# Kernel tuning notes

Measured on AMD Instinct MI355X. Metric: run time of the kernel, lower is better.

The kernel has to match this reference:

```python
import jax, jax.numpy as jnp
import numpy as np

N = 2048        # number of entities
D = 2048        # entity_dimensionality
HEADS = 16
HD = D // HEADS  # per-head dim = 128
ROUNDS = 2
LAYERS = 2


def setup_inputs() -> dict:
    key = jax.random.key(0)
    ks = jax.random.split(key, 12)
    s = 1.0 / np.sqrt(D)  # keep activations O(1)
    inp = {
        "entities": jax.random.normal(ks[0], (N, D), jnp.float32),
        "Wq": jax.random.normal(ks[1], (D, D), jnp.float32) * s,
        "bq": jnp.zeros((D,), jnp.float32),
        "Wk": jax.random.normal(ks[2], (D, D), jnp.float32) * s,
        "bk": jnp.zeros((D,), jnp.float32),
        "Wv": jax.random.normal(ks[3], (D, D), jnp.float32) * s,
        "bv": jnp.zeros((D,), jnp.float32),
        "W0": jax.random.normal(ks[4], (D, D), jnp.float32) * s,
        "b0": jnp.zeros((D,), jnp.float32),
        "W1": jax.random.normal(ks[5], (D, D), jnp.float32) * s,
        "b1": jnp.zeros((D,), jnp.float32),
    }
    return inp


def _linear(x, W, b):
    # torch nn.Linear: y = x @ W.T + b
    return x @ W.T + b


def _split_heads(x):
    # [N, D] -> [H, N, hd]
    return x.reshape(N, HEADS, HD).transpose(1, 0, 2)


def reference(entities, Wq, bq, Wk, bk, Wv, bv, W0, b0, W1, b1):
    scale = 1.0 / np.sqrt(HD)
    for _ in range(ROUNDS):
        q = _split_heads(_linear(entities, Wq, bq))  # [H, N, hd]
        k = _split_heads(_linear(entities, Wk, bk))
        v = _split_heads(_linear(entities, Wv, bv))
        scores = jnp.einsum('hqd,hkd->hqk', q, k) * scale  # [H, N, N]
        attn = jax.nn.softmax(scores, axis=-1)
        o = jnp.einsum('hqk,hkd->hqd', attn, v)            # [H, N, hd]
        o = o.transpose(1, 0, 2).reshape(N, D)             # merge heads
        o = jax.nn.relu(_linear(o, W0, b0))
        o = jax.nn.relu(_linear(o, W1, b1))
        entities = entities + o  # residual=True
    return entities
```

## Files before the change

kernel.cpp:

```cpp
#include <hip/hip_runtime.h>
#include <stdint.h>

#define DIM   2048
#define NENT  2048
#define NHEAD 16
#define HD    128

typedef unsigned short u16;
typedef u16   u16x4  __attribute__((ext_vector_type(4)));
typedef u16   u16x8  __attribute__((ext_vector_type(8)));
typedef float f32x4  __attribute__((ext_vector_type(4)));
typedef float f32x16 __attribute__((ext_vector_type(16)));
typedef __bf16 bf16x8 __attribute__((ext_vector_type(8)));

#define MFMA16(a, b, c) __builtin_amdgcn_mfma_f32_16x16x32_bf16((a), (b), (c), 0, 0, 0)
#define MFMA32(a, b, c) __builtin_amdgcn_mfma_f32_32x32x16_bf16((a), (b), (c), 0, 0, 0)

#define SMUL 0.12751743f

__device__ __forceinline__ u16 f2b(float f) {
  union { float f; unsigned int u; } x; x.f = f;
  unsigned int r = x.u + 0x7FFFu + ((x.u >> 16) & 1u);
  return (u16)(r >> 16);
}
__device__ __forceinline__ float b2f(u16 b) {
  union { unsigned int u; float f; } x; x.u = ((unsigned int)b) << 16;
  return x.f;
}
__device__ __forceinline__ unsigned int cvtpk(float a, float b) {
  unsigned int r;
  asm("v_cvt_pk_bf16_f32 %0, %1, %2" : "=v"(r) : "v"(a), "v"(b));
  return r;
}
__device__ __forceinline__ float exp2_fast(float x) {
  float r;
  asm("v_exp_f32 %0, %1" : "=v"(r) : "v"(x));
  return r;
}

__device__ __forceinline__ void async16(const void* g, void* l) {
  __builtin_amdgcn_global_load_lds(
      (const __attribute__((address_space(1))) unsigned int*)(uintptr_t)g,
      (__attribute__((address_space(3))) unsigned int*)(uintptr_t)l, 16, 0, 0);
}

__global__ void __launch_bounds__(256) conv6_k(
    const float* __restrict__ s0, const float* __restrict__ s1,
    const float* __restrict__ s2, const float* __restrict__ s3,
    const float* __restrict__ s4, const float* __restrict__ s5,
    u16* __restrict__ d0, u16* __restrict__ d1, u16* __restrict__ d2,
    u16* __restrict__ d3, u16* __restrict__ d4, u16* __restrict__ d5) {
  int sel = blockIdx.y;
  const float* s = sel == 0 ? s0 : sel == 1 ? s1 : sel == 2 ? s2
                 : sel == 3 ? s3 : sel == 4 ? s4 : s5;
  u16* d = sel == 0 ? d0 : sel == 1 ? d1 : sel == 2 ? d2
         : sel == 3 ? d3 : sel == 4 ? d4 : d5;
  int i = blockIdx.x * 256 + threadIdx.x;
  float4 v = ((const float4*)s)[i];
  u16x4 o;
  o.x = f2b(v.x); o.y = f2b(v.y); o.z = f2b(v.z); o.w = f2b(v.w);
  *(u16x4*)(d + (size_t)i * 4) = o;
}

template <int MODE>
__device__ __forceinline__ void gemm128_body(
    u16* sbuf,
    const u16* __restrict__ A, const u16* __restrict__ Bw,
    const float* __restrict__ bias, u16* __restrict__ C,
    int brow0, int bcol0, int kbase, int NT, float oscale) {
  u16* lA = sbuf;
  u16* lB = sbuf + 8192;
  const int tid = threadIdx.x;
  const int lane = tid & 63, w = tid >> 6;
  const int wr = w >> 1, wc = w & 1;
  const int l15 = lane & 15;
  const int koff = (lane >> 4) * 8;
  const int swz = (l15 & 7) << 3;

  f32x4 acc[4][4];
#pragma unroll
  for (int m = 0; m < 4; m++)
#pragma unroll
    for (int n = 0; n < 4; n++) acc[m][n] = (f32x4)0.f;

  const int lr = w * 8 + (lane >> 3);
  const int scol = ((lane & 7) ^ (lr & 7)) * 8;

#pragma unroll 1
  for (int kt = 0; kt < NT; kt++) {
    const int colg = kbase + kt * 64 + scol;
#pragma unroll
    for (int i = 0; i < 4; i++) {
      async16(A + (size_t)(brow0 + i * 32 + lr) * DIM + colg,
              lA + i * 2048 + w * 512);
      async16(Bw + (size_t)(bcol0 + i * 32 + lr) * DIM + colg,
              lB + i * 2048 + w * 512);
    }
    __syncthreads();
#pragma unroll
    for (int kk = 0; kk < 2; kk++) {
      bf16x8 af[4], bfr[4];
#pragma unroll
      for (int m = 0; m < 4; m++)
        af[m] = *(const bf16x8*)(lA + (wr * 64 + m * 16 + l15) * 64 +
                                 ((kk * 32 + koff) ^ swz));
#pragma unroll
      for (int n = 0; n < 4; n++)
        bfr[n] = *(const bf16x8*)(lB + (wc * 64 + n * 16 + l15) * 64 +
                                  ((kk * 32 + koff) ^ swz));
#pragma unroll
      for (int m = 0; m < 4; m++)
#pragma unroll
        for (int n = 0; n < 4; n++)
          acc[m][n] = MFMA16(af[m], bfr[n], acc[m][n]);
    }
    __syncthreads();
  }

  if (MODE == 2) {
    u16* arena = sbuf + w * 4096;
#pragma unroll
    for (int n = 0; n < 4; n++) {
      int c_loc = n * 16 + l15;
      float bv = bias[bcol0 + wc * 64 + c_loc];
#pragma unroll
      for (int m = 0; m < 4; m++)
#pragma unroll
        for (int r = 0; r < 4; r++) {
          int r_loc = m * 16 + (lane >> 4) * 4 + r;
          arena[c_loc * 64 + (r_loc ^ ((c_loc & 7) * 8))] =
              f2b(acc[m][n][r] + bv);
        }
    }
    __syncthreads();
    const int h = (bcol0 + wc * 64) >> 7;
    const int d0 = (bcol0 + wc * 64) & 127;
    const int R0 = brow0 + wr * 64;
    u16* vbase = C + (size_t)h * HD * NENT + R0;
#pragma unroll
    for (int it = 0; it < 8; it++) {
      int d_loc = it * 8 + (lane >> 3);
      int r0 = (lane & 7) * 8;
      u16x8 val = *(const u16x8*)(arena + d_loc * 64 + (r0 ^ ((d_loc & 7) * 8)));
      *(u16x8*)(vbase + (size_t)(d0 + d_loc) * NENT + r0) = val;
    }
    return;
  }

#pragma unroll
  for (int n = 0; n < 4; n++) {
    int col = bcol0 + wc * 64 + n * 16 + l15;
    float bv = (MODE == 0) ? bias[col] : 0.f;
#pragma unroll
    for (int m = 0; m < 4; m++) {
#pragma unroll
      for (int r = 0; r < 4; r++) {
        int row = brow0 + wr * 64 + m * 16 + (lane >> 4) * 4 + r;
        float val = acc[m][n][r] + bv;
        if (MODE == 0) val *= oscale;
        C[(size_t)row * DIM + col] = f2b(val);
      }
    }
  }
}

__global__ void __launch_bounds__(256, 3) gemm128_qkv_k(
    const u16* __restrict__ A,
    const u16* __restrict__ Bq, const u16* __restrict__ Bk, const u16* __restrict__ Bv,
    const float* __restrict__ bq, const float* __restrict__ bk, const float* __restrict__ bv,
    u16* __restrict__ q, u16* __restrict__ k, u16* __restrict__ vt) {
  __shared__ u16 sbuf[2 * 128 * 64];
  int x = blockIdx.x & 7;
  int j = blockIdx.x >> 3;
  int bn48 = x * 6 + j % 6;
  int bm = j / 6;
  int sel = bn48 >> 4, bnn = bn48 & 15;
  if (sel == 2) {
    gemm128_body<2>(sbuf, A, Bv, bv, vt, bm * 128, bnn * 128, 0, 32, 1.f);
  } else {
    const u16* B = sel == 0 ? Bq : Bk;
    const float* bias = sel == 0 ? bq : bk;
    u16* Cc = sel == 0 ? q : k;
    gemm128_body<0>(sbuf, A, B, bias, Cc, bm * 128, bnn * 128, 0, 32,
                    sel == 0 ? SMUL : 1.f);
  }
}

__global__ void __launch_bounds__(256, 3) gemm128_sk3_k(
    const u16* __restrict__ A, const u16* __restrict__ Bw,
    u16* __restrict__ p0, u16* __restrict__ p1, u16* __restrict__ p2) {
  __shared__ u16 sbuf[2 * 128 * 64];
  int x = blockIdx.x & 7;
  int j = blockIdx.x >> 3;
  int rem = j % 6;
  int bn = 2 * x + (rem & 1);
  int sk = rem >> 1;
  int bm = j / 6;
  u16* part = sk == 0 ? p0 : (sk == 1 ? p1 : p2);
  int nt = (sk == 2) ? 10 : 11;
  gemm128_body<1>(sbuf, A, Bw, nullptr, part, bm * 128, bn * 128,
                  sk * 11 * 64, nt, 1.f);
}

template <int RESID>
__global__ void __launch_bounds__(256) reduce3_k(
    const u16* __restrict__ p0, const u16* __restrict__ p1,
    const u16* __restrict__ p2,
    const float* __restrict__ bias, const float* __restrict__ resid,
    float* __restrict__ outf, u16* __restrict__ outb) {
  int i = blockIdx.x * 256 + threadIdx.x;
  u16x8 a0 = ((const u16x8*)p0)[i];
  u16x8 a1 = ((const u16x8*)p1)[i];
  u16x8 a2 = ((const u16x8*)p2)[i];
  size_t base = (size_t)i * 8;
  int col = (int)(base & (DIM - 1));
  u16x8 ob;
  float of[8];
#pragma unroll
  for (int j = 0; j < 8; j++) {
    float s = b2f(a0[j]) + b2f(a1[j]) + b2f(a2[j]) + bias[col + j];
    s = fmaxf(s, 0.f);
    if (RESID) {
      float o = resid[base + j] + s;
      of[j] = o;
      ob[j] = f2b(o);
    } else {
      ob[j] = f2b(s);
    }
  }
  *(u16x8*)(outb + base) = ob;
  if (RESID) {
#pragma unroll
    for (int j = 0; j < 8; j++) outf[base + j] = of[j];
  }
}

__global__ void __launch_bounds__(256, 2) attn_k(
    const u16* __restrict__ q, const u16* __restrict__ kmat,
    const u16* __restrict__ vt, u16* __restrict__ oz0, u16* __restrict__ oz1,
    float* __restrict__ ml) {
  const int h = blockIdx.x, qb = blockIdx.y, kvs = blockIdx.z;
  u16* __restrict__ oz = kvs ? oz1 : oz0;
  __shared__ u16 lK[2][64 * 128];
  __shared__ u16 lV[2][128 * 64];
  const int tid = threadIdx.x, lane = tid & 63, w = tid >> 6;
  const int l31 = lane & 31, hl = lane >> 5;
  const int r4 = lane >> 4, r8 = lane >> 3;
  const int c16e = (lane & 15) * 8, c8e = (lane & 7) * 8;
  const int swz = (l31 & 7) << 3;
  const u16* vhead = vt + (size_t)h * HD * NENT;
  const int kv0 = kvs * (NENT / 2);

  const int qrow = qb * 128 + w * 32 + l31;
  const u16* qptr = q + (size_t)qrow * DIM + h * HD + hl * 8;
  bf16x8 qf[8];
#pragma unroll
  for (int ks = 0; ks < 8; ks++)
    qf[ks] = *(const bf16x8*)(qptr + ks * 16);

  auto stageKV = [&](int kt, int buf) {
    const size_t krow0 = (size_t)kv0 + kt * 64;
#pragma unroll
    for (int c = 0; c < 4; c++) {
      int ch = w * 4 + c;
      int krow = ch * 4 + r4;
      async16(kmat + (krow0 + krow) * DIM + h * HD + (c16e ^ ((krow & 7) << 3)),
              lK[buf] + ch * 512);
      int vrow = ch * 8 + r8;
      async16(vhead + (size_t)vrow * NENT + krow0 + (c8e ^ ((r8 & 7) << 3)),
              lV[buf] + ch * 512);
    }
  };

  f32x16 Oacc[4];
#pragma unroll
  for (int dt = 0; dt < 4; dt++) Oacc[dt] = (f32x16)0.f;
  float m_i = -1e30f, l_i = 0.f;

  stageKV(0, 0);
  int cur = 0;

#pragma unroll 1
  for (int kt = 0; kt < NENT / 2 / 64; kt++) {
    __syncthreads();
    if (kt + 1 < NENT / 2 / 64) stageKV(kt + 1, cur ^ 1);
    const u16* Kc = lK[cur];
    const u16* Vc = lV[cur];

    f32x16 sA = (f32x16)0.f, sB = (f32x16)0.f;
#pragma unroll
    for (int ks = 0; ks < 8; ks++) {
      bf16x8 a0 = *(const bf16x8*)(Kc + l31 * 128 + ((ks * 16 + hl * 8) ^ swz));
      sA = MFMA32(a0, qf[ks], sA);
      bf16x8 a1 = *(const bf16x8*)(Kc + (32 + l31) * 128 + ((ks * 16 + hl * 8) ^ swz));
      sB = MFMA32(a1, qf[ks], sB);
    }

    float pmax = sA[0];
#pragma unroll
    for (int i = 1; i < 16; i++) pmax = fmaxf(pmax, sA[i]);
#pragma unroll
    for (int i = 0; i < 16; i++) pmax = fmaxf(pmax, sB[i]);
    pmax = fmaxf(pmax, __shfl_xor(pmax, 32));
    bool resc = __any(pmax > m_i + 8.f);
    float corr = 1.f;
    if (resc) {
      float mn = fmaxf(m_i, pmax);
      corr = exp2_fast(m_i - mn);
      m_i = mn;
    }
    float ls = 0.f;
#pragma unroll
    for (int i = 0; i < 16; i++) { sA[i] = exp2_fast(sA[i] - m_i); ls += sA[i]; }
#pragma unroll
    for (int i = 0; i < 16; i++) { sB[i] = exp2_fast(sB[i] - m_i); ls += sB[i]; }
    l_i = l_i * corr + ls;
    if (resc) {
#pragma unroll
      for (int r = 0; r < 16; r++) {
        int qo = hl * 4 + (r & 3) + 8 * (r >> 2);
        float cr = __shfl(corr, qo);
        Oacc[0][r] *= cr; Oacc[1][r] *= cr; Oacc[2][r] *= cr; Oacc[3][r] *= cr;
      }
    }

#pragma unroll
    for (int ks = 0; ks < 4; ks++) {
      const f32x16& p = (ks < 2) ? sA : sB;
      const int E = ((2 * ks) & 3) * 4;
      const int Od = ((2 * ks + 1) & 3) * 4;
      unsigned int e0 = cvtpk(p[E + 0], p[E + 1]);
      unsigned int e1 = cvtpk(p[E + 2], p[E + 3]);
      unsigned int o0 = cvtpk(p[Od + 0], p[Od + 1]);
      unsigned int o1 = cvtpk(p[Od + 2], p[Od + 3]);
      asm volatile("v_permlane32_swap_b32 %0, %1" : "+v"(e0), "+v"(o0));
      asm volatile("v_permlane32_swap_b32 %0, %1" : "+v"(e1), "+v"(o1));
      union { unsigned int u[4]; bf16x8 v; } pk;
      pk.u[0] = e0; pk.u[1] = e1; pk.u[2] = o0; pk.u[3] = o1;
#pragma unroll
      for (int dt = 0; dt < 4; dt++) {
        bf16x8 b = *(const bf16x8*)(Vc + (dt * 32 + l31) * 64 +
                                    ((ks * 16 + hl * 8) ^ swz));
        Oacc[dt] = MFMA32(pk.v, b, Oacc[dt]);
      }
    }
    cur ^= 1;
  }

  float lt = l_i + __shfl_xor(l_i, 32);
  if (hl == 0) {
    float* mlp = ml + ((size_t)(kvs * NHEAD + h) * NENT + qrow) * 2;
    mlp[0] = m_i;
    mlp[1] = lt;
  }
#pragma unroll
  for (int r = 0; r < 16; r++) {
    int row = qb * 128 + w * 32 + hl * 4 + (r & 3) + 8 * (r >> 2);
#pragma unroll
    for (int dt = 0; dt < 4; dt++)
      oz[(size_t)row * DIM + h * HD + dt * 32 + l31] = f2b(Oacc[dt][r]);
  }
}

__global__ void __launch_bounds__(256) combine_k(
    const u16* __restrict__ O0, const u16* __restrict__ O1,
    const float* __restrict__ ml, u16* __restrict__ o) {
  int i = blockIdx.x * 256 + threadIdx.x;
  size_t base = (size_t)i * 8;
  int row = (int)(base >> 11);
  int h = ((int)base & (DIM - 1)) >> 7;
  const float* p0 = ml + ((size_t)h * NENT + row) * 2;
  const float* p1 = ml + ((size_t)(NHEAD + h) * NENT + row) * 2;
  float m0 = p0[0], l0 = p0[1];
  float m1 = p1[0], l1 = p1[1];
  float M = fmaxf(m0, m1);
  float w0 = exp2_fast(m0 - M), w1 = exp2_fast(m1 - M);
  float inv = 1.f / (l0 * w0 + l1 * w1);
  w0 *= inv; w1 *= inv;
  u16x8 a = ((const u16x8*)O0)[i], b = ((const u16x8*)O1)[i];
  u16x8 r;
#pragma unroll
  for (int j = 0; j < 8; j++) r[j] = f2b(b2f(a[j]) * w0 + b2f(b[j]) * w1);
  ((u16x8*)o)[i] = r;
}

extern "C" void kernel_launch(void* const* d_in, const int* in_sizes, int n_in,
                              void* d_out, int out_size, void* d_ws, size_t ws_size,
                              hipStream_t stream) {
  const float* ent_in = (const float*)d_in[0];
  const float* Wq = (const float*)d_in[1];
  const float* bq = (const float*)d_in[2];
  const float* Wk = (const float*)d_in[3];
  const float* bk = (const float*)d_in[4];
  const float* Wv = (const float*)d_in[5];
  const float* bv = (const float*)d_in[6];
  const float* W0 = (const float*)d_in[7];
  const float* b0 = (const float*)d_in[8];
  const float* W1 = (const float*)d_in[9];
  const float* b1 = (const float*)d_in[10];
  float* out = (float*)d_out;

  char* ws = (char*)d_ws;
  const size_t SZ = (size_t)DIM * DIM * 2;
  u16* wqb = (u16*)ws; ws += SZ;
  u16* wkb = (u16*)ws; ws += SZ;
  u16* wvb = (u16*)ws; ws += SZ;
  u16* w0b = (u16*)ws; ws += SZ;
  u16* w1b = (u16*)ws; ws += SZ;
  u16* entb = (u16*)ws; ws += SZ;
  u16* qb_ = (u16*)ws; ws += SZ;
  u16* kb_ = (u16*)ws; ws += SZ;
  u16* vb_ = (u16*)ws; ws += SZ;
  u16* vtb = (u16*)ws; ws += SZ;
  u16* ob_ = (u16*)ws; ws += SZ;
  u16* h1b = (u16*)ws; ws += SZ;

  conv6_k<<<dim3(4096, 6), 256, 0, stream>>>(Wq, Wk, Wv, W0, W1, ent_in,
                                             wqb, wkb, wvb, w0b, w1b, entb);

  for (int r = 0; r < 2; r++) {
    const float* cur = r ? (const float*)out : ent_in;
    gemm128_qkv_k<<<768, 256, 0, stream>>>(entb, wqb, wkb, wvb, bq, bk, bv,
                                           qb_, kb_, vtb);
    attn_k<<<dim3(16, 16, 2), 256, 0, stream>>>(qb_, kb_, vtb, vb_, h1b,
                                                (float*)entb);
    combine_k<<<2048, 256, 0, stream>>>(vb_, h1b, (const float*)entb, ob_);
    gemm128_sk3_k<<<768, 256, 0, stream>>>(ob_, w0b, entb, qb_, kb_);
    reduce3_k<0><<<2048, 256, 0, stream>>>(entb, qb_, kb_, b0, nullptr,
                                           nullptr, h1b);
    gemm128_sk3_k<<<768, 256, 0, stream>>>(h1b, w1b, entb, qb_, kb_);
    reduce3_k<1><<<2048, 256, 0, stream>>>(entb, qb_, kb_, b1, cur,
                                           out, entb);
  }
}
```

Measured before the change: 356.7 us.

## Split attention KV into three chunks, single-buffer LDS, raise occupancy

The attention kernel now splits the key/value range into three chunks (704/704/640 rows) instead of two, giving 768 blocks, and drops the double-buffered LDS staging in favour of a single buffer so three blocks can fit per CU. MFMA sections are wrapped in s_setprio to favour matrix issue across co-resident waves. The combine kernel merges three partial outputs, reusing ob_ as both the third partial and the output in place. The gain relies on occupancy and more blocks hiding load latency. The cost is losing the explicit prefetch overlap, adding an extra sync per tile, and more partial-output traffic in the combine step.

```diff
diff --git a/kernel.cpp b/kernel.cpp
--- a/kernel.cpp
+++ b/kernel.cpp
@@ -235,21 +235,22 @@
   }
 }
 
-__global__ void __launch_bounds__(256, 2) attn_k(
+__global__ void __launch_bounds__(256, 3) attn_k(
     const u16* __restrict__ q, const u16* __restrict__ kmat,
     const u16* __restrict__ vt, u16* __restrict__ oz0, u16* __restrict__ oz1,
-    float* __restrict__ ml) {
+    u16* __restrict__ oz2, float* __restrict__ ml) {
   const int h = blockIdx.x, qb = blockIdx.y, kvs = blockIdx.z;
-  u16* __restrict__ oz = kvs ? oz1 : oz0;
-  __shared__ u16 lK[2][64 * 128];
-  __shared__ u16 lV[2][128 * 64];
+  u16* __restrict__ oz = kvs == 0 ? oz0 : (kvs == 1 ? oz1 : oz2);
+  const int NT = (kvs == 2) ? 10 : 11;
+  const int kv0 = kvs * 704;
+  __shared__ u16 lK[64 * 128];
+  __shared__ u16 lV[128 * 64];
   const int tid = threadIdx.x, lane = tid & 63, w = tid >> 6;
   const int l31 = lane & 31, hl = lane >> 5;
   const int r4 = lane >> 4, r8 = lane >> 3;
   const int c16e = (lane & 15) * 8, c8e = (lane & 7) * 8;
   const int swz = (l31 & 7) << 3;
   const u16* vhead = vt + (size_t)h * HD * NENT;
-  const int kv0 = kvs * (NENT / 2);
 
   const int qrow = qb * 128 + w * 32 + l31;
   const u16* qptr = q + (size_t)qrow * DIM + h * HD + hl * 8;
@@ -258,43 +259,36 @@
   for (int ks = 0; ks < 8; ks++)
     qf[ks] = *(const bf16x8*)(qptr + ks * 16);
 
-  auto stageKV = [&](int kt, int buf) {
+  f32x16 Oacc[4];
+#pragma unroll
+  for (int dt = 0; dt < 4; dt++) Oacc[dt] = (f32x16)0.f;
+  float m_i = -1e30f, l_i = 0.f;
+
+#pragma unroll 1
+  for (int kt = 0; kt < NT; kt++) {
     const size_t krow0 = (size_t)kv0 + kt * 64;
 #pragma unroll
     for (int c = 0; c < 4; c++) {
       int ch = w * 4 + c;
       int krow = ch * 4 + r4;
       async16(kmat + (krow0 + krow) * DIM + h * HD + (c16e ^ ((krow & 7) << 3)),
-              lK[buf] + ch * 512);
+              lK + ch * 512);
       int vrow = ch * 8 + r8;
       async16(vhead + (size_t)vrow * NENT + krow0 + (c8e ^ ((r8 & 7) << 3)),
-              lV[buf] + ch * 512);
-    }
-  };
-
-  f32x16 Oacc[4];
-#pragma unroll
-  for (int dt = 0; dt < 4; dt++) Oacc[dt] = (f32x16)0.f;
-  float m_i = -1e30f, l_i = 0.f;
-
-  stageKV(0, 0);
-  int cur = 0;
-
-#pragma unroll 1
-  for (int kt = 0; kt < NENT / 2 / 64; kt++) {
+              lV + ch * 512);
+    }
     __syncthreads();
-    if (kt + 1 < NENT / 2 / 64) stageKV(kt + 1, cur ^ 1);
-    const u16* Kc = lK[cur];
-    const u16* Vc = lV[cur];
 
     f32x16 sA = (f32x16)0.f, sB = (f32x16)0.f;
+    __builtin_amdgcn_s_setprio(1);
 #pragma unroll
     for (int ks = 0; ks < 8; ks++) {
-      bf16x8 a0 = *(const bf16x8*)(Kc + l31 * 128 + ((ks * 16 + hl * 8) ^ swz));
+      bf16x8 a0 = *(const bf16x8*)(lK + l31 * 128 + ((ks * 16 + hl * 8) ^ swz));
       sA = MFMA32(a0, qf[ks], sA);
-      bf16x8 a1 = *(const bf16x8*)(Kc + (32 + l31) * 128 + ((ks * 16 + hl * 8) ^ swz));
+      bf16x8 a1 = *(const bf16x8*)(lK + (32 + l31) * 128 + ((ks * 16 + hl * 8) ^ swz));
       sB = MFMA32(a1, qf[ks], sB);
     }
+    __builtin_amdgcn_s_setprio(0);
 
     float pmax = sA[0];
 #pragma unroll
@@ -324,6 +318,7 @@
       }
     }
 
+    __builtin_amdgcn_s_setprio(1);
 #pragma unroll
     for (int ks = 0; ks < 4; ks++) {
       const f32x16& p = (ks < 2) ? sA : sB;
@@ -339,12 +334,13 @@
       pk.u[0] = e0; pk.u[1] = e1; pk.u[2] = o0; pk.u[3] = o1;
 #pragma unroll
       for (int dt = 0; dt < 4; dt++) {
-        bf16x8 b = *(const bf16x8*)(Vc + (dt * 32 + l31) * 64 +
+        bf16x8 b = *(const bf16x8*)(lV + (dt * 32 + l31) * 64 +
                                     ((ks * 16 + hl * 8) ^ swz));
         Oacc[dt] = MFMA32(pk.v, b, Oacc[dt]);
       }
     }
-    cur ^= 1;
+    __builtin_amdgcn_s_setprio(0);
+    __syncthreads();
   }
 
   float lt = l_i + __shfl_xor(l_i, 32);
@@ -362,8 +358,9 @@
   }
 }
 
-__global__ void __launch_bounds__(256) combine_k(
+__global__ void __launch_bounds__(256) combine3_k(
     const u16* __restrict__ O0, const u16* __restrict__ O1,
+    const u16* __restrict__ O2,
     const float* __restrict__ ml, u16* __restrict__ o) {
   int i = blockIdx.x * 256 + threadIdx.x;
   size_t base = (size_t)i * 8;
@@ -371,16 +368,20 @@
   int h = ((int)base & (DIM - 1)) >> 7;
   const float* p0 = ml + ((size_t)h * NENT + row) * 2;
   const float* p1 = ml + ((size_t)(NHEAD + h) * NENT + row) * 2;
+  const float* p2 = ml + ((size_t)(2 * NHEAD + h) * NENT + row) * 2;
   float m0 = p0[0], l0 = p0[1];
   float m1 = p1[0], l1 = p1[1];
-  float M = fmaxf(m0, m1);
-  float w0 = exp2_fast(m0 - M), w1 = exp2_fast(m1 - M);
-  float inv = 1.f / (l0 * w0 + l1 * w1);
-  w0 *= inv; w1 *= inv;
+  float m2 = p2[0], l2 = p2[1];
+  float M = fmaxf(fmaxf(m0, m1), m2);
+  float w0 = exp2_fast(m0 - M), w1 = exp2_fast(m1 - M), w2 = exp2_fast(m2 - M);
+  float inv = 1.f / (l0 * w0 + l1 * w1 + l2 * w2);
+  w0 *= inv; w1 *= inv; w2 *= inv;
   u16x8 a = ((const u16x8*)O0)[i], b = ((const u16x8*)O1)[i];
+  u16x8 c = ((const u16x8*)O2)[i];
   u16x8 r;
 #pragma unroll
-  for (int j = 0; j < 8; j++) r[j] = f2b(b2f(a[j]) * w0 + b2f(b[j]) * w1);
+  for (int j = 0; j < 8; j++)
+    r[j] = f2b(b2f(a[j]) * w0 + b2f(b[j]) * w1 + b2f(c[j]) * w2);
   ((u16x8*)o)[i] = r;
 }
 
@@ -422,9 +423,10 @@
     const float* cur = r ? (const float*)out : ent_in;
     gemm128_qkv_k<<<768, 256, 0, stream>>>(entb, wqb, wkb, wvb, bq, bk, bv,
                                            qb_, kb_, vtb);
-    attn_k<<<dim3(16, 16, 2), 256, 0, stream>>>(qb_, kb_, vtb, vb_, h1b,
+    attn_k<<<dim3(16, 16, 3), 256, 0, stream>>>(qb_, kb_, vtb, vb_, h1b, ob_,
                                                 (float*)entb);
-    combine_k<<<2048, 256, 0, stream>>>(vb_, h1b, (const float*)entb, ob_);
+    combine3_k<<<2048, 256, 0, stream>>>(vb_, h1b, ob_, (const float*)entb,
+                                         ob_);
     gemm128_sk3_k<<<768, 256, 0, stream>>>(ob_, w0b, entb, qb_, kb_);
     reduce3_k<0><<<2048, 256, 0, stream>>>(entb, qb_, kb_, b0, nullptr,
                                            nullptr, h1b);
```

Measured after the change: 434.9 us. 21.9% more time.
